# Optimization experiments

Measured on AMD Instinct MI355X. Metric: run time of the kernel, lower is better.

Reference implementation:

```python
import jax, jax.numpy as jnp
import numpy as np

N_BINS = 256
HOP = 80


def _gru(xs, Wih, Whh, bih, bhh, reverse=False):
    """Single-layer unidirectional GRU, PyTorch gate layout (r, z, n).
    xs: (T, B, I); Wih: (3H, I); Whh: (3H, H). Returns (T, B, H)."""
    H = Whh.shape[1]
    gi = jnp.einsum('tbi,gi->tbg', xs, Wih) + bih  # precompute input projections

    def step(h, gi_t):
        gh = h @ Whh.T + bhh
        ir, iz, inn = jnp.split(gi_t, 3, axis=-1)
        hr, hz, hn = jnp.split(gh, 3, axis=-1)
        r = jax.nn.sigmoid(ir + hr)
        z = jax.nn.sigmoid(iz + hz)
        n = jnp.tanh(inn + r * hn)
        h_new = (1.0 - z) * n + z * h
        return h_new, h_new

    h0 = jnp.zeros((xs.shape[1], H), xs.dtype)
    _, ys = jax.lax.scan(step, h0, gi, reverse=reverse)
    return ys


def _quantize(w):
    # continuous [-1, 1] -> bin index in [0, N_BINS-1]
    return jnp.clip(jnp.floor((w + 1.0) * (N_BINS / 2)), 0, N_BINS - 1).astype(jnp.int32)


def _forward(x, y, p):
    # --- encode: 2-layer bidirectional GRU over mel frames ---
    c = x
    for l in ('m0', 'm1'):
        f = _gru(c, p[l + 'f_Wih'], p[l + 'f_Whh'], p[l + 'f_bih'], p[l + 'f_bhh'])
        bwd = _gru(c, p[l + 'b_Wih'], p[l + 'b_Whh'], p[l + 'b_bih'], p[l + 'b_bhh'], reverse=True)
        c = jnp.concatenate([f, bwd], axis=-1)  # (t_m, b, 2*dim_enc)
    # nearest-neighbor upsample in time (matches F.interpolate default 'nearest')
    c = jnp.repeat(c, HOP, axis=0)  # (t_w, b, 2*dim_enc)

    # --- teacher forcing: shift waveform right, vectorize via embedding ---
    b = x.shape[1]
    w = jnp.concatenate([jnp.zeros((1, b), y.dtype), y[:-1]], axis=0)
    e = p['E'][_quantize(w)]  # (t_w, b, dim_vec)

    # --- wav GRU + projection + GELU ---
    o = _gru(jnp.concatenate([e, c], axis=-1), p['w_Wih'], p['w_Whh'], p['w_bih'], p['w_bhh'])
    o = jax.nn.gelu(o @ p['Wp'].T + p['bp'], approximate=False)  # (t_w, b, dim_proj)

    # --- categorical neg log prob over quantized targets ---
    logits = o @ p['Wd'].T + p['bd']  # (t_w, b, N_BINS)
    logp = jax.nn.log_softmax(logits, axis=-1)
    tgt = _quantize(y)
    nll = -jnp.mean(jnp.take_along_axis(logp, tgt[..., None], axis=-1))
    return nll


def setup_inputs() -> dict:
    key = jax.random.key(0)
    ks = iter(jax.random.split(key, 64))

    def rn(shape, s=0.08):
        return jax.random.normal(next(ks), shape, jnp.float32) * s

    t_m, b, dm = 32, 4, 80
    de, dv, dd, dp = 128, 256, 896, 512
    d = {}
    d['x'] = jax.random.normal(next(ks), (t_m, b, dm), jnp.float32)
    d['y'] = jax.random.uniform(next(ks), (t_m * HOP, b), jnp.float32, minval=-1.0, maxval=1.0)
    for name, i in [('m0f', dm), ('m0b', dm), ('m1f', 2 * de), ('m1b', 2 * de)]:
        d[name + '_Wih'] = rn((3 * de, i))
        d[name + '_Whh'] = rn((3 * de, de))
        d[name + '_bih'] = rn((3 * de,))
        d[name + '_bhh'] = rn((3 * de,))
    d['w_Wih'] = rn((3 * dd, 2 * de + dv))
    d['w_Whh'] = rn((3 * dd, dd))
    d['w_bih'] = rn((3 * dd,))
    d['w_bhh'] = rn((3 * dd,))
    d['Wp'] = rn((dp, dd))
    d['bp'] = rn((dp,))
    d['E'] = rn((N_BINS, dv))
    d['Wd'] = rn((N_BINS, dp))
    d['bd'] = rn((N_BINS,))
    return d


def reference(x, y, m0f_Wih, m0f_Whh, m0f_bih, m0f_bhh, m0b_Wih, m0b_Whh, m0b_bih, m0b_bhh,
              m1f_Wih, m1f_Whh, m1f_bih, m1f_bhh, m1b_Wih, m1b_Whh, m1b_bih, m1b_bhh,
              w_Wih, w_Whh, w_bih, w_bhh, Wp, bp, E, Wd, bd):
    p = dict(m0f_Wih=m0f_Wih, m0f_Whh=m0f_Whh, m0f_bih=m0f_bih, m0f_bhh=m0f_bhh,
             m0b_Wih=m0b_Wih, m0b_Whh=m0b_Whh, m0b_bih=m0b_bih, m0b_bhh=m0b_bhh,
             m1f_Wih=m1f_Wih, m1f_Whh=m1f_Whh, m1f_bih=m1f_bih, m1f_bhh=m1f_bhh,
             m1b_Wih=m1b_Wih, m1b_Whh=m1b_Whh, m1b_bih=m1b_bih, m1b_bhh=m1b_bhh,
             w_Wih=w_Wih, w_Whh=w_Whh, w_bih=w_bih, w_bhh=w_bhh,
             Wp=Wp, bp=bp, E=E, Wd=Wd, bd=bd)
    return _forward(x, y, p)
```

## Files before the change

### kernel.cpp

```cpp
#include <hip/hip_runtime.h>
#include <stdint.h>
#include <math.h>

typedef __attribute__((ext_vector_type(8))) short bf16x8;
typedef __attribute__((ext_vector_type(4))) float f32x4;
typedef __attribute__((ext_vector_type(4))) unsigned int u32x4;

#define BATCH 4
#define T_M 32
#define DE 128
#define T_W 2560
#define NWG 28

__device__ __forceinline__ float b2f(unsigned short h) {
  return __uint_as_float(((unsigned int)h) << 16);
}
__device__ __forceinline__ unsigned short f2b(float f) {
  unsigned int u = __float_as_uint(f);
  u = u + 0x7fffu + ((u >> 16) & 1u);
  return (unsigned short)(u >> 16);
}
__device__ __forceinline__ float blo(unsigned int u){ return __uint_as_float(u << 16); }
__device__ __forceinline__ float bhi(unsigned int u){ return __uint_as_float(u & 0xffff0000u); }
__device__ __forceinline__ float sigm(float x){
  return __builtin_amdgcn_rcpf(1.f + __expf(-x));
}
__device__ __forceinline__ float tanh_fast(float x){
  float x2 = fminf(fmaxf(x + x, -30.f), 30.f);
  return 1.f - 2.f * __builtin_amdgcn_rcpf(__expf(x2) + 1.f);
}
__device__ __forceinline__ float gelu_exact(float x){ return 0.5f * x * (1.f + erff(x * 0.70710678118654752f)); }

__global__ __launch_bounds__(256) void k_cast(const float* __restrict__ src,
                                              unsigned short* __restrict__ dst, int n)
{
  int i = blockIdx.x * 256 + threadIdx.x;
  if (i < n) dst[i] = f2b(src[i]);
}

__global__ __launch_bounds__(256) void k_prep_whh(const float* __restrict__ whh,
                                                  unsigned short* __restrict__ out)
{
  int idx = blockIdx.x * 256 + threadIdx.x;
  if (idx >= 224 * 28 * 512) return;
  int j    = idx & 7;
  int r16  = (idx >> 3) & 15;
  int quad = (idx >> 7) & 3;
  int kc   = (idx >> 9) % 28;
  int G    = (idx >> 9) / 28;
  unsigned short val = 0;
  if (r16 < 12) {
    int row = (r16 >> 2) * 896 + G * 4 + (r16 & 3);
    int col = kc * 32 + quad * 8 + j;
    val = f2b(whh[(size_t)row * 896 + col]);
  }
  out[idx] = val;
}

__global__ __launch_bounds__(384) void k_gi_enc(
    const float* __restrict__ in, const float* __restrict__ Wih,
    const float* __restrict__ bih, float* __restrict__ out, int K)
{
  __shared__ float in_s[256];
  int tb = blockIdx.x;
  for (int i = threadIdx.x; i < K; i += 384) in_s[i] = in[tb * K + i];
  __syncthreads();
  int row = threadIdx.x;
  float acc = bih[row];
  const float* wr = Wih + row * K;
  for (int k = 0; k < K; ++k) acc += in_s[k] * wr[k];
  out[tb * 384 + row] = acc;
}

__global__ __launch_bounds__(512) void k_scan_enc(
    const float* __restrict__ gi_f, const float* __restrict__ gi_b,
    const float* __restrict__ whh_f, const float* __restrict__ bhh_f,
    const float* __restrict__ whh_b, const float* __restrict__ bhh_b,
    float* __restrict__ c_out)
{
  const int dir = blockIdx.x, tid = threadIdx.x;
  const float* gi  = dir ? gi_b  : gi_f;
  const float* whh = dir ? whh_b : whh_f;
  const float* bhh = dir ? bhh_b : bhh_f;
  __shared__ unsigned short h_s[BATCH][DE + 8];
  __shared__ float gh_s[384][4];
  __shared__ float bhh_s[384];
  for (int i = tid; i < 384; i += 512) bhh_s[i] = bhh[i];
  for (int i = tid; i < BATCH * (DE + 8); i += 512) ((unsigned short*)h_s)[i] = 0;
  __syncthreads();
  for (int s = 0; s < T_M; ++s) {
    int t = dir ? (T_M - 1 - s) : s;
    #pragma unroll
    for (int k3 = 0; k3 < 3; ++k3) {
      int d = tid + 512 * k3;
      int row = d >> 2, b = d & 3;
      const float* wr = whh + row * DE;
      float acc = 0.f;
      for (int j = 0; j < DE; j += 8) {
        float4 w0 = *(const float4*)(wr + j);
        float4 w1 = *(const float4*)(wr + j + 4);
        uint4  hv = *(const uint4*)&h_s[b][j];
        acc += w0.x * blo(hv.x) + w0.y * bhi(hv.x) + w0.z * blo(hv.y) + w0.w * bhi(hv.y);
        acc += w1.x * blo(hv.z) + w1.y * bhi(hv.z) + w1.z * blo(hv.w) + w1.w * bhi(hv.w);
      }
      gh_s[row][b] = acc + bhh_s[row];
    }
    __syncthreads();
    {
      int u = tid >> 2, b = tid & 3;
      const float* git = gi + (t * BATCH + b) * 384;
      float r = sigm(git[u] + gh_s[u][b]);
      float z = sigm(git[DE + u] + gh_s[DE + u][b]);
      float n = tanh_fast(git[2 * DE + u] + r * gh_s[2 * DE + u][b]);
      float hold = b2f(h_s[b][u]);
      float hnew = (1.f - z) * n + z * hold;
      c_out[(t * BATCH + b) * 256 + dir * DE + u] = hnew;
      h_s[b][u] = f2b(hnew);
    }
    __syncthreads();
  }
}

__global__ __launch_bounds__(256) void k_build_X(
    const float* __restrict__ y, const float* __restrict__ E,
    const float* __restrict__ c1, unsigned short* __restrict__ X)
{
  int t = blockIdx.x, c = threadIdx.x;
  int tm = t / 80;
  #pragma unroll
  for (int b = 0; b < BATCH; ++b) {
    float w = (t == 0) ? 0.f : y[(t - 1) * BATCH + b];
    int q = (int)floorf((w + 1.f) * 128.f);
    q = q < 0 ? 0 : (q > 255 ? 255 : q);
    unsigned short* xb = X + (size_t)(t * BATCH + b) * 512;
    xb[c]       = f2b(E[q * 256 + c]);
    xb[256 + c] = f2b(c1[(tm * BATCH + b) * 256 + c]);
  }
}

__global__ __launch_bounds__(256) void k_mgemm(
    const unsigned short* __restrict__ A, const unsigned short* __restrict__ B,
    const float* __restrict__ bias, void* __restrict__ C,
    int M, int N, int K, int act, int c_bf16, int swz)
{
  __shared__ unsigned short As[128][40];
  __shared__ unsigned short Bs[128][40];
  const int tid = threadIdx.x;
  const int m0 = blockIdx.x * 128, n0 = blockIdx.y * 128;
  const int lane = tid & 63, wave = tid >> 6;
  const int wy = wave >> 1, wx = wave & 1;
  const int row16 = lane & 15, quad = lane >> 4;
  const int sr = tid >> 1, sc = (tid & 1) * 16;
  f32x4 acc[4][4] = {};
  for (int kt = 0; kt < K; kt += 32) {
    uint4 av  = *(const uint4*)(A + (size_t)(m0 + sr) * K + kt + sc);
    uint4 av2 = *(const uint4*)(A + (size_t)(m0 + sr) * K + kt + sc + 8);
    uint4 bv  = *(const uint4*)(B + (size_t)(n0 + sr) * K + kt + sc);
    uint4 bv2 = *(const uint4*)(B + (size_t)(n0 + sr) * K + kt + sc + 8);
    __syncthreads();
    *(uint4*)&As[sr][sc] = av; *(uint4*)&As[sr][sc + 8] = av2;
    *(uint4*)&Bs[sr][sc] = bv; *(uint4*)&Bs[sr][sc + 8] = bv2;
    __syncthreads();
    bf16x8 af[4], bf[4];
    #pragma unroll
    for (int i = 0; i < 4; ++i) af[i] = *(const bf16x8*)&As[wy * 64 + i * 16 + row16][quad * 8];
    #pragma unroll
    for (int j = 0; j < 4; ++j) bf[j] = *(const bf16x8*)&Bs[wx * 64 + j * 16 + row16][quad * 8];
    #pragma unroll
    for (int i = 0; i < 4; ++i)
      #pragma unroll
      for (int j = 0; j < 4; ++j)
        acc[i][j] = __builtin_amdgcn_mfma_f32_16x16x32_bf16(af[i], bf[j], acc[i][j], 0, 0, 0);
  }
  #pragma unroll
  for (int i = 0; i < 4; ++i) {
    #pragma unroll
    for (int j = 0; j < 4; ++j) {
      int col = n0 + wx * 64 + j * 16 + row16;
      float bs = bias[col];
      #pragma unroll
      for (int r = 0; r < 4; ++r) {
        int row = m0 + wy * 64 + i * 16 + quad * 4 + r;
        float v = acc[i][j][r] + bs;
        if (act) v = gelu_exact(v);
        if (swz) {
          int t = row >> 2, b = row & 3;
          int g = col / 896, rem = col - g * 896;
          int G = rem >> 2, u = rem & 3;
          ((unsigned short*)C)[(size_t)(t * 224 + G) * 48 + g * 16 + b * 4 + u] = f2b(v);
        } else if (c_bf16) {
          ((unsigned short*)C)[(size_t)row * N + col] = f2b(v);
        } else {
          ((float*)C)[(size_t)row * N + col] = v;
        }
      }
    }
  }
}

__global__ __launch_bounds__(512, 1) void k_wav_rnn(
    const unsigned short* __restrict__ whh_p,
    const float* __restrict__ bhh,
    const unsigned short* __restrict__ gp_,
    unsigned int* __restrict__ hslots,
    unsigned int* __restrict__ O32)
{
  const int wg = blockIdx.x, tid = threadIdx.x;
  const int lane = tid & 63, wave = tid >> 6;
  const int G = wg * 8 + wave;

  __shared__ unsigned short h_lds[2][4][912];
  __shared__ float phh[8][3][4][4];

  const int r16 = lane & 15, quad = lane >> 4, bb = lane & 3;
  const int fu = (lane >> 2) & 3, fb = lane & 3;

  bf16x8 wf[28];
  {
    const bf16x8* W8 = (const bf16x8*)whh_p + (size_t)G * 28 * 64;
    #pragma unroll
    for (int kc = 0; kc < 28; ++kc)
      wf[kc] = W8[(kc * 4 + quad) * 16 + r16];
  }

  const float br_ = bhh[G * 4 + fu];
  const float bz_ = bhh[896 + G * 4 + fu];
  const float bn_ = bhh[1792 + G * 4 + fu];
  float hprev = 0.f;
  const unsigned short* gl0 = gp_ + (size_t)G * 48 + fb * 4 + fu;
  unsigned short cr = gl0[0], cz = gl0[16], cn = gl0[32];

  const int l56 = (lane < 56) ? lane : (lane - 56);
  const int p0 = wave * 112 + l56;
  const int p1 = p0 + 56;
  const int pb0 = p0 / 224, pG0 = p0 - pb0 * 224;
  const int pb1 = p1 / 224, pG1 = p1 - pb1 * 224;

  const unsigned long long base0 = (unsigned long long)hslots;
  const unsigned long long base1 = base0 + 14336ull;

  for (int t = 0; t < T_W; ++t) {
    const unsigned long long hb = (t & 1) ? base1 : base0;
    unsigned long long a0 = hb + ((unsigned long long)p0 << 4);
    unsigned long long a1 = hb + ((unsigned long long)p1 << 4);
    u32x4 s0, s1;
    const unsigned int tg = (unsigned int)t;
    unsigned int bad;
    do {
      asm volatile(
        "global_load_dwordx4 %0, %2, off sc0 sc1\n"
        "global_load_dwordx4 %1, %3, off sc0 sc1\n"
        "s_waitcnt vmcnt(0)"
        : "=&v"(s0), "=&v"(s1)
        : "v"(a0), "v"(a1)
        : "memory");
      bad = (s0.z ^ tg) | (s1.z ^ tg);
    } while (__any(bad != 0));

    int tn = (t + 1 < T_W) ? (t + 1) : t;
    const unsigned short* gp = gp_ + (size_t)tn * 10752 + G * 48 + fb * 4 + fu;
    unsigned short nr_ = gp[0], nz_ = gp[16], nn_ = gp[32];

    if (lane < 56) {
      *(uint2*)&h_lds[t & 1][pb0][pG0 * 4] = make_uint2(s0.x, s0.y);
      *(uint2*)&h_lds[t & 1][pb1][pG1 * 4] = make_uint2(s1.x, s1.y);
    }
    __syncthreads();

    f32x4 ac0 = {}, ac1 = {}, ac2 = {}, ac3 = {};
    #pragma unroll
    for (int kc = 0; kc < 28; kc += 4) {
      bf16x8 h0 = *(const bf16x8*)&h_lds[t & 1][bb][(kc + 0) * 32 + quad * 8];
      bf16x8 h1 = *(const bf16x8*)&h_lds[t & 1][bb][(kc + 1) * 32 + quad * 8];
      bf16x8 h2 = *(const bf16x8*)&h_lds[t & 1][bb][(kc + 2) * 32 + quad * 8];
      bf16x8 h3 = *(const bf16x8*)&h_lds[t & 1][bb][(kc + 3) * 32 + quad * 8];
      ac0 = __builtin_amdgcn_mfma_f32_16x16x32_bf16(wf[kc + 0], h0, ac0, 0, 0, 0);
      ac1 = __builtin_amdgcn_mfma_f32_16x16x32_bf16(wf[kc + 1], h1, ac1, 0, 0, 0);
      ac2 = __builtin_amdgcn_mfma_f32_16x16x32_bf16(wf[kc + 2], h2, ac2, 0, 0, 0);
      ac3 = __builtin_amdgcn_mfma_f32_16x16x32_bf16(wf[kc + 3], h3, ac3, 0, 0, 0);
    }
    f32x4 ac;
    ac[0] = ac0[0] + ac1[0] + ac2[0] + ac3[0];
    ac[1] = ac0[1] + ac1[1] + ac2[1] + ac3[1];
    ac[2] = ac0[2] + ac1[2] + ac2[2] + ac3[2];
    ac[3] = ac0[3] + ac1[3] + ac2[3] + ac3[3];

    if (r16 < 4 && quad < 3)
      *(f32x4*)&phh[wave][quad][r16][0] = ac;
    asm volatile("s_waitcnt lgkmcnt(0)" ::: "memory");

    float pr = phh[wave][0][fb][fu];
    float pz = phh[wave][1][fb][fu];
    float pn = phh[wave][2][fb][fu];
    float r = sigm(b2f(cr) + br_ + pr);
    float z = sigm(b2f(cz) + bz_ + pz);
    float n = tanh_fast(b2f(cn) + bn_ + r * pn);
    float h = (1.f - z) * n + z * hprev;
    hprev = h;
    unsigned int hu = f2b(h);
    cr = nr_; cz = nz_; cn = nn_;

    int b = lane & 3;
    unsigned int u0v = (unsigned int)__shfl((int)hu, 0 + b);
    unsigned int u1v = (unsigned int)__shfl((int)hu, 4 + b);
    unsigned int u2v = (unsigned int)__shfl((int)hu, 8 + b);
    unsigned int u3v = (unsigned int)__shfl((int)hu, 12 + b);
    if (lane < 4) {
      u32x4 pkt;
      pkt.x = (u0v & 0xffffu) | (u1v << 16);
      pkt.y = (u2v & 0xffffu) | (u3v << 16);
      pkt.z = (unsigned int)(t + 1);
      pkt.w = 0u;
      unsigned long long sa = (((t + 1) & 1) ? base1 : base0)
                            + (unsigned long long)((b * 224 + G) << 4);
      asm volatile("global_store_dwordx4 %0, %1, off sc0 sc1"
                   :: "v"(sa), "v"(pkt) : "memory");
      *(uint2*)(O32 + (size_t)(t * 4 + b) * 448 + G * 2) = make_uint2(pkt.x, pkt.y);
    }
  }
}

__global__ __launch_bounds__(256) void k_nll(
    const float* __restrict__ logits, const float* __restrict__ y,
    float* __restrict__ acc)
{
  int wid = threadIdx.x >> 6, lane = threadIdx.x & 63;
  int row = blockIdx.x * 4 + wid;
  const float* lr = logits + (size_t)row * 256;
  float v0 = lr[lane], v1 = lr[lane + 64], v2 = lr[lane + 128], v3 = lr[lane + 192];
  float mx = fmaxf(fmaxf(v0, v1), fmaxf(v2, v3));
  for (int off = 32; off > 0; off >>= 1) mx = fmaxf(mx, __shfl_xor(mx, off));
  float se = __expf(v0 - mx) + __expf(v1 - mx) + __expf(v2 - mx) + __expf(v3 - mx);
  for (int off = 32; off > 0; off >>= 1) se += __shfl_xor(se, off);
  if (lane == 0) {
    float w = y[row];
    int q = (int)floorf((w + 1.f) * 128.f);
    q = q < 0 ? 0 : (q > 255 ? 255 : q);
    float contrib = (logf(se) + mx) - lr[q];
    atomicAdd(acc, contrib);
  }
}

__global__ void k_final(const float* __restrict__ acc, float* __restrict__ out) {
  out[0] = acc[0] * (1.f / 10240.f);
}

extern "C" void kernel_launch(void* const* d_in, const int* in_sizes, int n_in,
                              void* d_out, int out_size, void* d_ws, size_t ws_size,
                              hipStream_t stream)
{
  const float* x       = (const float*)d_in[0];
  const float* y       = (const float*)d_in[1];
  const float* m0f_Wih = (const float*)d_in[2];
  const float* m0f_Whh = (const float*)d_in[3];
  const float* m0f_bih = (const float*)d_in[4];
  const float* m0f_bhh = (const float*)d_in[5];
  const float* m0b_Wih = (const float*)d_in[6];
  const float* m0b_Whh = (const float*)d_in[7];
  const float* m0b_bih = (const float*)d_in[8];
  const float* m0b_bhh = (const float*)d_in[9];
  const float* m1f_Wih = (const float*)d_in[10];
  const float* m1f_Whh = (const float*)d_in[11];
  const float* m1f_bih = (const float*)d_in[12];
  const float* m1f_bhh = (const float*)d_in[13];
  const float* m1b_Wih = (const float*)d_in[14];
  const float* m1b_Whh = (const float*)d_in[15];
  const float* m1b_bih = (const float*)d_in[16];
  const float* m1b_bhh = (const float*)d_in[17];
  const float* w_Wih   = (const float*)d_in[18];
  const float* w_Whh   = (const float*)d_in[19];
  const float* w_bih   = (const float*)d_in[20];
  const float* w_bhh   = (const float*)d_in[21];
  const float* Wp      = (const float*)d_in[22];
  const float* bp      = (const float*)d_in[23];
  const float* E       = (const float*)d_in[24];
  const float* Wd      = (const float*)d_in[25];
  const float* bd      = (const float*)d_in[26];

  char* ws = (char*)d_ws;
  size_t off = 0;
  auto alloc = [&](size_t bytes) -> void* {
    void* p = ws + off;
    off += (bytes + 255) & ~(size_t)255;
    return p;
  };
  float*        nacc   = (float*)alloc(64);
  unsigned int* hslots = (unsigned int*)alloc(2 * 896 * 16);
  size_t misc_bytes = off;

  float* c0   = (float*)alloc((size_t)32 * 4 * 256 * 4);
  float* c1   = (float*)alloc((size_t)32 * 4 * 256 * 4);
  float* gi0f = (float*)alloc((size_t)32 * 4 * 384 * 4);
  float* gi0b = (float*)alloc((size_t)32 * 4 * 384 * 4);
  float* gi1f = (float*)alloc((size_t)32 * 4 * 384 * 4);
  float* gi1b = (float*)alloc((size_t)32 * 4 * 384 * 4);
  unsigned short* X     = (unsigned short*)alloc((size_t)10240 * 512 * 2);
  unsigned short* gpack = (unsigned short*)alloc((size_t)2560 * 224 * 48 * 2);
  unsigned int*   O32   = (unsigned int*)alloc((size_t)10240 * 448 * 4);
  unsigned short* O2    = (unsigned short*)alloc((size_t)10240 * 512 * 2);
  float*          LG    = (float*)alloc((size_t)10240 * 256 * 4);
  unsigned short* Wih_b = (unsigned short*)alloc((size_t)2688 * 512 * 2);
  unsigned short* Whh_p = (unsigned short*)alloc((size_t)224 * 28 * 512 * 2);
  unsigned short* Wp_b  = (unsigned short*)alloc((size_t)512 * 896 * 2);
  unsigned short* Wd_b  = (unsigned short*)alloc((size_t)256 * 512 * 2);

  hipMemsetAsync(d_ws, 0, misc_bytes, stream);

  k_cast<<<(2688 * 512 + 255) / 256, 256, 0, stream>>>(w_Wih, Wih_b, 2688 * 512);
  k_cast<<<(512 * 896 + 255) / 256, 256, 0, stream>>>(Wp, Wp_b, 512 * 896);
  k_cast<<<(256 * 512 + 255) / 256, 256, 0, stream>>>(Wd, Wd_b, 256 * 512);
  k_prep_whh<<<(224 * 28 * 512 + 255) / 256, 256, 0, stream>>>(w_Whh, Whh_p);

  k_gi_enc<<<128, 384, 0, stream>>>(x, m0f_Wih, m0f_bih, gi0f, 80);
  k_gi_enc<<<128, 384, 0, stream>>>(x, m0b_Wih, m0b_bih, gi0b, 80);
  k_scan_enc<<<2, 512, 0, stream>>>(gi0f, gi0b, m0f_Whh, m0f_bhh, m0b_Whh, m0b_bhh, c0);
  k_gi_enc<<<128, 384, 0, stream>>>(c0, m1f_Wih, m1f_bih, gi1f, 256);
  k_gi_enc<<<128, 384, 0, stream>>>(c0, m1b_Wih, m1b_bih, gi1b, 256);
  k_scan_enc<<<2, 512, 0, stream>>>(gi1f, gi1b, m1f_Whh, m1f_bhh, m1b_Whh, m1b_bhh, c1);

  k_build_X<<<2560, 256, 0, stream>>>(y, E, c1, X);
  k_mgemm<<<dim3(80, 21), 256, 0, stream>>>(X, Wih_b, w_bih, (void*)gpack,
                                            10240, 2688, 512, 0, 1, 1);

  k_wav_rnn<<<NWG, 512, 0, stream>>>(Whh_p, w_bhh, gpack, hslots, O32);

  k_mgemm<<<dim3(80, 4), 256, 0, stream>>>((const unsigned short*)O32, Wp_b, bp,
                                           (void*)O2, 10240, 512, 896, 1, 1, 0);
  k_mgemm<<<dim3(80, 2), 256, 0, stream>>>(O2, Wd_b, bd, (void*)LG,
                                           10240, 256, 512, 0, 0, 0);
  k_nll<<<2560, 256, 0, stream>>>(LG, y, nacc);
  k_final<<<1, 1, 0, stream>>>(nacc, (float*)d_out);
}
```

Baseline: 5.992 ms.

## Spread wav GRU over more workgroups and fuse embedding gather into input GEMM

The recurrent wav GRU kernel now runs 56 workgroups of 4 waves instead of 28 of 8. Each thread polls four hidden-state slots and sleeps briefly between failed polls, and the per-step cross-workgroup sync now involves twice as many participants. The separate k_build_X kernel and its large X buffer are removed. The input-projection GEMM now gathers embedding rows and encoder context directly from bf16 copies, computing the quantized index per row. The change aims to cut per-step latency and the memory traffic of materialising X, at the cost of a wider spin barrier and extra small cast launches.

```diff
diff --git a/kernel.cpp b/kernel.cpp
--- a/kernel.cpp
+++ b/kernel.cpp
@@ -10,7 +10,7 @@
 #define T_M 32
 #define DE 128
 #define T_W 2560
-#define NWG 28
+#define NWG 56
 
 __device__ __forceinline__ float b2f(unsigned short h) {
   return __uint_as_float(((unsigned int)h) << 16);
@@ -121,27 +121,12 @@
   }
 }
 
-__global__ __launch_bounds__(256) void k_build_X(
-    const float* __restrict__ y, const float* __restrict__ E,
-    const float* __restrict__ c1, unsigned short* __restrict__ X)
-{
-  int t = blockIdx.x, c = threadIdx.x;
-  int tm = t / 80;
-  #pragma unroll
-  for (int b = 0; b < BATCH; ++b) {
-    float w = (t == 0) ? 0.f : y[(t - 1) * BATCH + b];
-    int q = (int)floorf((w + 1.f) * 128.f);
-    q = q < 0 ? 0 : (q > 255 ? 255 : q);
-    unsigned short* xb = X + (size_t)(t * BATCH + b) * 512;
-    xb[c]       = f2b(E[q * 256 + c]);
-    xb[256 + c] = f2b(c1[(tm * BATCH + b) * 256 + c]);
-  }
-}
-
 __global__ __launch_bounds__(256) void k_mgemm(
     const unsigned short* __restrict__ A, const unsigned short* __restrict__ B,
     const float* __restrict__ bias, void* __restrict__ C,
-    int M, int N, int K, int act, int c_bf16, int swz)
+    int M, int N, int K, int act, int c_bf16, int swz, int afuse,
+    const unsigned short* __restrict__ Eb, const unsigned short* __restrict__ c1b,
+    const float* __restrict__ yw)
 {
   __shared__ unsigned short As[128][40];
   __shared__ unsigned short Bs[128][40];
@@ -151,10 +136,28 @@
   const int wy = wave >> 1, wx = wave & 1;
   const int row16 = lane & 15, quad = lane >> 4;
   const int sr = tid >> 1, sc = (tid & 1) * 16;
+  const unsigned short* arow0 = nullptr;
+  const unsigned short* arow1 = nullptr;
+  if (afuse) {
+    int row = m0 + sr, tt = row >> 2, b = row & 3;
+    float w = (tt == 0) ? 0.f : yw[(tt - 1) * 4 + b];
+    int q = (int)floorf((w + 1.f) * 128.f);
+    q = q < 0 ? 0 : (q > 255 ? 255 : q);
+    arow0 = Eb + q * 256;
+    arow1 = c1b + ((tt / 80) * 4 + b) * 256;
+  }
   f32x4 acc[4][4] = {};
   for (int kt = 0; kt < K; kt += 32) {
-    uint4 av  = *(const uint4*)(A + (size_t)(m0 + sr) * K + kt + sc);
-    uint4 av2 = *(const uint4*)(A + (size_t)(m0 + sr) * K + kt + sc + 8);
+    uint4 av, av2;
+    if (afuse) {
+      int kk = kt + sc;
+      const unsigned short* src = (kk < 256) ? (arow0 + kk) : (arow1 + kk - 256);
+      av  = *(const uint4*)src;
+      av2 = *(const uint4*)(src + 8);
+    } else {
+      av  = *(const uint4*)(A + (size_t)(m0 + sr) * K + kt + sc);
+      av2 = *(const uint4*)(A + (size_t)(m0 + sr) * K + kt + sc + 8);
+    }
     uint4 bv  = *(const uint4*)(B + (size_t)(n0 + sr) * K + kt + sc);
     uint4 bv2 = *(const uint4*)(B + (size_t)(n0 + sr) * K + kt + sc + 8);
     __syncthreads();
@@ -198,7 +201,7 @@
   }
 }
 
-__global__ __launch_bounds__(512, 1) void k_wav_rnn(
+__global__ __launch_bounds__(256, 1) void k_wav_rnn(
     const unsigned short* __restrict__ whh_p,
     const float* __restrict__ bhh,
     const unsigned short* __restrict__ gp_,
@@ -207,10 +210,10 @@
 {
   const int wg = blockIdx.x, tid = threadIdx.x;
   const int lane = tid & 63, wave = tid >> 6;
-  const int G = wg * 8 + wave;
+  const int G = wg * 4 + wave;
 
   __shared__ unsigned short h_lds[2][4][912];
-  __shared__ float phh[8][3][4][4];
+  __shared__ float phh[4][3][4][4];
 
   const int r16 = lane & 15, quad = lane >> 4, bb = lane & 3;
   const int fu = (lane >> 2) & 3, fb = lane & 3;
@@ -230,11 +233,12 @@
   const unsigned short* gl0 = gp_ + (size_t)G * 48 + fb * 4 + fu;
   unsigned short cr = gl0[0], cz = gl0[16], cn = gl0[32];
 
-  const int l56 = (lane < 56) ? lane : (lane - 56);
-  const int p0 = wave * 112 + l56;
-  const int p1 = p0 + 56;
+  const int p0 = tid, p1 = tid + 256, p2 = tid + 512;
+  const int p3 = (tid < 128) ? tid + 768 : tid;
   const int pb0 = p0 / 224, pG0 = p0 - pb0 * 224;
   const int pb1 = p1 / 224, pG1 = p1 - pb1 * 224;
+  const int pb2 = p2 / 224, pG2 = p2 - pb2 * 224;
+  const int pb3 = p3 / 224, pG3 = p3 - pb3 * 224;
 
   const unsigned long long base0 = (unsigned long long)hslots;
   const unsigned long long base1 = base0 + 14336ull;
@@ -243,28 +247,33 @@
     const unsigned long long hb = (t & 1) ? base1 : base0;
     unsigned long long a0 = hb + ((unsigned long long)p0 << 4);
     unsigned long long a1 = hb + ((unsigned long long)p1 << 4);
-    u32x4 s0, s1;
+    unsigned long long a2 = hb + ((unsigned long long)p2 << 4);
+    unsigned long long a3 = hb + ((unsigned long long)p3 << 4);
+    u32x4 s0, s1, s2, s3;
     const unsigned int tg = (unsigned int)t;
-    unsigned int bad;
-    do {
+    for (;;) {
       asm volatile(
-        "global_load_dwordx4 %0, %2, off sc0 sc1\n"
-        "global_load_dwordx4 %1, %3, off sc0 sc1\n"
+        "global_load_dwordx4 %0, %4, off sc0 sc1\n"
+        "global_load_dwordx4 %1, %5, off sc0 sc1\n"
+        "global_load_dwordx4 %2, %6, off sc0 sc1\n"
+        "global_load_dwordx4 %3, %7, off sc0 sc1\n"
         "s_waitcnt vmcnt(0)"
-        : "=&v"(s0), "=&v"(s1)
-        : "v"(a0), "v"(a1)
+        : "=&v"(s0), "=&v"(s1), "=&v"(s2), "=&v"(s3)
+        : "v"(a0), "v"(a1), "v"(a2), "v"(a3)
         : "memory");
-      bad = (s0.z ^ tg) | (s1.z ^ tg);
-    } while (__any(bad != 0));
+      unsigned int bad = (s0.z ^ tg) | (s1.z ^ tg) | (s2.z ^ tg) | (s3.z ^ tg);
+      if (!__any(bad != 0)) break;
+      __builtin_amdgcn_s_sleep(1);
+    }
 
     int tn = (t + 1 < T_W) ? (t + 1) : t;
     const unsigned short* gp = gp_ + (size_t)tn * 10752 + G * 48 + fb * 4 + fu;
     unsigned short nr_ = gp[0], nz_ = gp[16], nn_ = gp[32];
 
-    if (lane < 56) {
-      *(uint2*)&h_lds[t & 1][pb0][pG0 * 4] = make_uint2(s0.x, s0.y);
-      *(uint2*)&h_lds[t & 1][pb1][pG1 * 4] = make_uint2(s1.x, s1.y);
-    }
+    *(uint2*)&h_lds[t & 1][pb0][pG0 * 4] = make_uint2(s0.x, s0.y);
+    *(uint2*)&h_lds[t & 1][pb1][pG1 * 4] = make_uint2(s1.x, s1.y);
+    *(uint2*)&h_lds[t & 1][pb2][pG2 * 4] = make_uint2(s2.x, s2.y);
+    *(uint2*)&h_lds[t & 1][pb3][pG3 * 4] = make_uint2(s3.x, s3.y);
     __syncthreads();
 
     f32x4 ac0 = {}, ac1 = {}, ac2 = {}, ac3 = {};
@@ -394,7 +403,8 @@
   float* gi0b = (float*)alloc((size_t)32 * 4 * 384 * 4);
   float* gi1f = (float*)alloc((size_t)32 * 4 * 384 * 4);
   float* gi1b = (float*)alloc((size_t)32 * 4 * 384 * 4);
-  unsigned short* X     = (unsigned short*)alloc((size_t)10240 * 512 * 2);
+  unsigned short* Eb    = (unsigned short*)alloc((size_t)256 * 256 * 2);
+  unsigned short* c1b   = (unsigned short*)alloc((size_t)32 * 4 * 256 * 2);
   unsigned short* gpack = (unsigned short*)alloc((size_t)2560 * 224 * 48 * 2);
   unsigned int*   O32   = (unsigned int*)alloc((size_t)10240 * 448 * 4);
   unsigned short* O2    = (unsigned short*)alloc((size_t)10240 * 512 * 2);
@@ -409,6 +419,7 @@
   k_cast<<<(2688 * 512 + 255) / 256, 256, 0, stream>>>(w_Wih, Wih_b, 2688 * 512);
   k_cast<<<(512 * 896 + 255) / 256, 256, 0, stream>>>(Wp, Wp_b, 512 * 896);
   k_cast<<<(256 * 512 + 255) / 256, 256, 0, stream>>>(Wd, Wd_b, 256 * 512);
+  k_cast<<<(256 * 256 + 255) / 256, 256, 0, stream>>>(E, Eb, 256 * 256);
   k_prep_whh<<<(224 * 28 * 512 + 255) / 256, 256, 0, stream>>>(w_Whh, Whh_p);
 
   k_gi_enc<<<128, 384, 0, stream>>>(x, m0f_Wih, m0f_bih, gi0f, 80);
@@ -417,17 +428,19 @@
   k_gi_enc<<<128, 384, 0, stream>>>(c0, m1f_Wih, m1f_bih, gi1f, 256);
   k_gi_enc<<<128, 384, 0, stream>>>(c0, m1b_Wih, m1b_bih, gi1b, 256);
   k_scan_enc<<<2, 512, 0, stream>>>(gi1f, gi1b, m1f_Whh, m1f_bhh, m1b_Whh, m1b_bhh, c1);
-
-  k_build_X<<<2560, 256, 0, stream>>>(y, E, c1, X);
-  k_mgemm<<<dim3(80, 21), 256, 0, stream>>>(X, Wih_b, w_bih, (void*)gpack,
-                                            10240, 2688, 512, 0, 1, 1);
-
-  k_wav_rnn<<<NWG, 512, 0, stream>>>(Whh_p, w_bhh, gpack, hslots, O32);
+  k_cast<<<(32 * 4 * 256 + 255) / 256, 256, 0, stream>>>(c1, c1b, 32 * 4 * 256);
+
+  k_mgemm<<<dim3(80, 21), 256, 0, stream>>>(nullptr, Wih_b, w_bih, (void*)gpack,
+                                            10240, 2688, 512, 0, 1, 1, 1, Eb, c1b, y);
+
+  k_wav_rnn<<<NWG, 256, 0, stream>>>(Whh_p, w_bhh, gpack, hslots, O32);
 
   k_mgemm<<<dim3(80, 4), 256, 0, stream>>>((const unsigned short*)O32, Wp_b, bp,
-                                           (void*)O2, 10240, 512, 896, 1, 1, 0);
+                                           (void*)O2, 10240, 512, 896, 1, 1, 0, 0,
+                                           nullptr, nullptr, nullptr);
   k_mgemm<<<dim3(80, 2), 256, 0, stream>>>(O2, Wd_b, bd, (void*)LG,
-                                           10240, 256, 512, 0, 0, 0);
+                                           10240, 256, 512, 0, 0, 0, 0,
+                                           nullptr, nullptr, nullptr);
   k_nll<<<2560, 256, 0, stream>>>(LG, y, nacc);
   k_final<<<1, 1, 0, stream>>>(nacc, (float*)d_out);
 }
```

New measurement: 6.020 ms. No clear change (+0.5%).
